# Optimization experiments

Hardware: AMD Instinct MI355X
Metric: run time of the kernel (lower is better)

The kernel has to match this reference:

```python
import jax, jax.numpy as jnp
import numpy as np

D = 512          # input_size (feature dim)
C = 100          # num_classes
N = 2048         # test samples
ALPHA = 0.5      # regularization mixing parameter
SHRINK = 1e-4    # shrinkage_param


def setup_inputs() -> dict:
    key = jax.random.key(0)
    k1, k2, k3, k4, k5 = jax.random.split(key, 5)
    X = jax.random.normal(k1, (N, D), dtype=jnp.float32)
    muK = jax.random.normal(k2, (C, D), dtype=jnp.float32)
    # Per-class covariances: PSD, well-conditioned (like fitted streaming covariances)
    A = jax.random.normal(k3, (C, D, D), dtype=jnp.float32) * 0.05
    SigmaK = jnp.einsum('cij,ckj->cik', A, A) + 0.1 * jnp.eye(D, dtype=jnp.float32)
    B = jax.random.normal(k4, (D, D), dtype=jnp.float32) * 0.05
    Sigma = B @ B.T + 0.1 * jnp.eye(D, dtype=jnp.float32)
    # class counts (all > 0 so every class is active)
    cK = jax.random.uniform(k5, (C,), dtype=jnp.float32, minval=1.0, maxval=1000.0)
    return {"X": X, "muK": muK, "SigmaK": SigmaK, "Sigma": Sigma, "cK": cK}


def reference(X, muK, SigmaK, Sigma, cK):
    # RegSigmaK[k] = alpha * SigmaK[k] + (1-alpha) * Sigma           [C, D, D]
    RegSigmaK = ALPHA * SigmaK + (1.0 - ALPHA) * Sigma[None, :, :]
    # priors (classes with zero count get prior 1, then are masked to -inf below)
    s = jnp.sum(cK)
    prior = jnp.where(cK == 0, 1.0, cK / s)                          # [C]
    # Lambda[k] = pinv((1-sh) * RegSigmaK[k] + sh * I)               [C, D, D]
    eye = jnp.eye(D, dtype=RegSigmaK.dtype)
    Lambda = jnp.linalg.pinv((1.0 - SHRINK) * RegSigmaK + SHRINK * eye)
    # 0.5 * log ||RegSigmaK[k]||_F  (torch.norm default = Frobenius)
    half_lognorm = 0.5 * jnp.log(jnp.linalg.norm(RegSigmaK, axis=(1, 2)))  # [C]
    # batched Mahalanobis quadratic form: (x - mu_k)^T Lambda_k (x - mu_k)
    diff = X[:, None, :] - muK[None, :, :]                           # [N, C, D]
    quad = jnp.einsum('ncd,cde,nce->nc', diff, Lambda, diff)         # [N, C]
    scores = jnp.log(prior)[None, :] - half_lognorm[None, :] - 0.5 * quad
    scores = jnp.where((cK == 0)[None, :], -jnp.inf, scores)
    return scores
```

## Files before the change

kernel.cpp:

```cpp
#include <hip/hip_runtime.h>
#include <math.h>

#define DIM 512
#define NCLS 100
#define NS 2048
#define DD (DIM*DIM)
#define SHRINKV 1e-4f

typedef short bf16x8 __attribute__((ext_vector_type(8)));
typedef short s16x4 __attribute__((ext_vector_type(4)));
typedef float f32x4 __attribute__((ext_vector_type(4)));

static __device__ __forceinline__ short f2bf(float f) {
  unsigned int u = __float_as_uint(f);
  u += 0x7FFFu + ((u >> 16) & 1u);
  return (short)(u >> 16);
}

__global__ __launch_bounds__(256) void prep_kernel(const float* __restrict__ SigmaK,
                                                   const float* __restrict__ Sigma,
                                                   float* __restrict__ M,
                                                   float* __restrict__ aux) {
  int b = blockIdx.x;
  int k = b >> 2, chunk = b & 3;
  const float* Sk = SigmaK + (size_t)k * DD;
  float* Mk = M + (size_t)k * DD;
  int base0 = chunk << 16;
  float fro = 0.f;
  const float oms = 1.0f - SHRINKV;
  for (int it = 0; it < 64; ++it) {
    int idx = base0 + (it << 10) + (threadIdx.x << 2);
    float4 a = *(const float4*)(Sk + idx);
    float4 g = *(const float4*)(Sigma + idx);
    int r = idx >> 9, c = idx & 511;
    float4 reg;
    reg.x = 0.5f*(a.x + g.x); reg.y = 0.5f*(a.y + g.y);
    reg.z = 0.5f*(a.z + g.z); reg.w = 0.5f*(a.w + g.w);
    fro += reg.x*reg.x + reg.y*reg.y + reg.z*reg.z + reg.w*reg.w;
    float4 m;
    m.x = oms*reg.x + ((r == c + 0) ? SHRINKV : 0.f);
    m.y = oms*reg.y + ((r == c + 1) ? SHRINKV : 0.f);
    m.z = oms*reg.z + ((r == c + 2) ? SHRINKV : 0.f);
    m.w = oms*reg.w + ((r == c + 3) ? SHRINKV : 0.f);
    *(float4*)(Mk + idx) = m;
  }
  __shared__ float red[4];
  int lane = threadIdx.x & 63, w = threadIdx.x >> 6;
  for (int o = 32; o > 0; o >>= 1) fro += __shfl_down(fro, o);
  if (lane == 0) red[w] = fro;
  __syncthreads();
  if (threadIdx.x == 0) atomicAdd(&aux[1 + k], red[0] + red[1] + red[2] + red[3]);
}

__global__ __launch_bounds__(256) void fdt_kernel(float* __restrict__ M,
                                                  short* __restrict__ Wb, int p) {
  __shared__ float Llds[64 * 68];
  __shared__ float invT[64 * 68];
  __shared__ float TA[2][64 * 68];
  int kcls = blockIdx.x;
  float* Mk = M + (size_t)kcls * DD;
  short* Wk = Wb + (size_t)kcls * DD;
  int tid = threadIdx.x, lane = tid & 63, wv = tid >> 6;
  int ty = tid >> 4, tx = tid & 15;
  int sr = tid >> 2, sq = (tid & 3) << 4;
  int p0 = p << 6;
  if (wv == 0) {
    float row[64];
    const float* src = Mk + (size_t)(p0 + lane) * DIM + p0;
    #pragma unroll
    for (int c4 = 0; c4 < 64; c4 += 4) {
      float4 v = *(const float4*)(src + c4);
      row[c4] = v.x; row[c4+1] = v.y; row[c4+2] = v.z; row[c4+3] = v.w;
    }
    #pragma unroll
    for (int j = 0; j < 64; ++j) {
      float diagv = __shfl(row[j], j);
      float dv = sqrtf(diagv);
      float rinv = 1.0f / dv;
      float myLj = row[j] * rinv;
      row[j] = myLj;
      #pragma unroll
      for (int c = j + 1; c < 64; ++c)
        row[c] = fmaf(-myLj, __shfl(myLj, c), row[c]);
    }
    #pragma unroll
    for (int c = 0; c < 64; ++c)
      Llds[lane * 68 + c] = (c <= lane) ? row[c] : 0.f;
  }
  __syncthreads();
  if (wv == 0) {
    float w[64];
    #pragma unroll
    for (int r = 0; r < 64; ++r) {
      float s = 0.f;
      #pragma unroll
      for (int kk = 0; kk + 4 <= r; kk += 4) {
        float4 lv = *(const float4*)(Llds + r*68 + kk);
        s += lv.x*w[kk] + lv.y*w[kk+1] + lv.z*w[kk+2] + lv.w*w[kk+3];
      }
      #pragma unroll
      for (int kk = r & ~3; kk < r; ++kk) s += Llds[r*68 + kk] * w[kk];
      float rhs = ((r == lane) ? 1.0f : 0.0f) - s;
      w[r] = rhs / Llds[r*68 + r];
    }
    #pragma unroll
    for (int r = 0; r < 64; ++r) {
      Mk[(size_t)(p0 + r)*DIM + p0 + lane] = w[r];
      Wk[(size_t)(p0 + r)*DIM + p0 + lane] = f2bf(w[r]);
      invT[lane*68 + r] = w[r];
    }
  } else if (p < 7) {
    int w1 = wv - 1;
    int r0 = (w1 == 0) ? 0 : (w1 == 1 ? 22 : 43);
    int r1 = (w1 == 0) ? 22 : (w1 == 1 ? 43 : 64);
    const float* ab = Mk + ((size_t)((p + 1) << 6)) * DIM + p0;
    for (int row = r0; row < r1; ++row)
      TA[0][lane*68 + row] = ab[(size_t)row * DIM + lane];
  }
  __syncthreads();
  int cur = 0;
  for (int i = p + 1; i < 8; ++i) {
    if (i + 1 < 8) {
      const float* a = Mk + (size_t)(((i + 1) << 6) + sr)*DIM + p0 + sq;
      #pragma unroll
      for (int t4 = 0; t4 < 4; ++t4) {
        float4 va = *(const float4*)(a + 4*t4);
        TA[cur^1][(sq+4*t4+0)*68+sr]=va.x; TA[cur^1][(sq+4*t4+1)*68+sr]=va.y;
        TA[cur^1][(sq+4*t4+2)*68+sr]=va.z; TA[cur^1][(sq+4*t4+3)*68+sr]=va.w;
      }
    }
    float acc[4][4];
    #pragma unroll
    for (int a2 = 0; a2 < 4; ++a2)
      #pragma unroll
      for (int b2 = 0; b2 < 4; ++b2) acc[a2][b2] = 0.f;
    #pragma unroll 16
    for (int m = 0; m < 64; ++m) {
      float4 av = *(const float4*)(TA[cur] + m*68 + (ty << 2));
      float4 bv = *(const float4*)(invT + m*68 + (tx << 2));
      float a4[4] = {av.x, av.y, av.z, av.w};
      float b4[4] = {bv.x, bv.y, bv.z, bv.w};
      #pragma unroll
      for (int ir = 0; ir < 4; ++ir)
        #pragma unroll
        for (int ic = 0; ic < 4; ++ic) acc[ir][ic] += a4[ir] * b4[ic];
    }
    #pragma unroll
    for (int q = 0; q < 4; ++q) {
      float4 v; v.x = acc[q][0]; v.y = acc[q][1]; v.z = acc[q][2]; v.w = acc[q][3];
      *(float4*)(Mk + (size_t)((i << 6) + (ty << 2) + q)*DIM + p0 + (tx << 2)) = v;
    }
    __syncthreads();
    cur ^= 1;
  }
}

__global__ __launch_bounds__(256) void syrk_kernel(float* __restrict__ M, int p) {
  __shared__ float TA[64 * 68];
  __shared__ float TB[64 * 68];
  int n = 7 - p;
  int T = n * (n + 1) / 2;
  int cls = blockIdx.x / T;
  int t = blockIdx.x % T;
  int bi = 0;
  while (t > bi) { t -= bi + 1; ++bi; }
  int i = p + 1 + bi, j = p + 1 + t;
  float* Mk = M + (size_t)cls * DD;
  int tid = threadIdx.x;
  int ty = tid >> 4, tx = tid & 15;
  int sr = tid >> 2, sq = (tid & 3) << 4;
  {
    const float* a = Mk + (size_t)((i << 6) + sr)*DIM + (p << 6) + sq;
    const float* b = Mk + (size_t)((j << 6) + sr)*DIM + (p << 6) + sq;
    #pragma unroll
    for (int t4 = 0; t4 < 4; ++t4) {
      float4 va = *(const float4*)(a + 4*t4);
      TA[(sq+4*t4+0)*68+sr]=va.x; TA[(sq+4*t4+1)*68+sr]=va.y;
      TA[(sq+4*t4+2)*68+sr]=va.z; TA[(sq+4*t4+3)*68+sr]=va.w;
      float4 vb = *(const float4*)(b + 4*t4);
      TB[(sq+4*t4+0)*68+sr]=vb.x; TB[(sq+4*t4+1)*68+sr]=vb.y;
      TB[(sq+4*t4+2)*68+sr]=vb.z; TB[(sq+4*t4+3)*68+sr]=vb.w;
    }
  }
  __syncthreads();
  float acc[4][4];
  #pragma unroll
  for (int a = 0; a < 4; ++a)
    #pragma unroll
    for (int b = 0; b < 4; ++b) acc[a][b] = 0.f;
  #pragma unroll 16
  for (int m = 0; m < 64; ++m) {
    float4 av = *(const float4*)(TA + m*68 + (ty << 2));
    float4 bv = *(const float4*)(TB + m*68 + (tx << 2));
    float a4[4] = {av.x, av.y, av.z, av.w};
    float b4[4] = {bv.x, bv.y, bv.z, bv.w};
    #pragma unroll
    for (int ir = 0; ir < 4; ++ir)
      #pragma unroll
      for (int ic = 0; ic < 4; ++ic) acc[ir][ic] += a4[ir] * b4[ic];
  }
  #pragma unroll
  for (int q = 0; q < 4; ++q) {
    float* dst = Mk + (size_t)((i << 6) + (ty << 2) + q)*DIM + (j << 6) + (tx << 2);
    float4 v = *(const float4*)dst;
    v.x -= acc[q][0]; v.y -= acc[q][1]; v.z -= acc[q][2]; v.w -= acc[q][3];
    *(float4*)dst = v;
  }
}

__global__ __launch_bounds__(256) void colsweep_kernel(float* __restrict__ M,
                                                       short* __restrict__ Wb) {
  __shared__ float TL[2][64 * 68];
  __shared__ float TW[2][64 * 68];
  int cls = blockIdx.x / 7;
  int j = blockIdx.x % 7;
  float* Mk = M + (size_t)cls * DD;
  short* Wk = Wb + (size_t)cls * DD;
  int tid = threadIdx.x;
  int ty = tid >> 4, tx = tid & 15;
  int sr = tid >> 2, sq = (tid & 3) << 4;
  for (int i = j + 1; i < 8; ++i) {
    auto stageLW = [&](int k, int buf) {
      const float* a = Mk + (size_t)((i << 6) + sr)*DIM + (k << 6) + sq;
      const float* b = Mk + (size_t)((j << 6) + sr)*DIM + (k << 6) + sq;
      #pragma unroll
      for (int t4 = 0; t4 < 4; ++t4) {
        float4 va = *(const float4*)(a + 4*t4);
        TL[buf][(sq+4*t4+0)*68+sr]=va.x; TL[buf][(sq+4*t4+1)*68+sr]=va.y;
        TL[buf][(sq+4*t4+2)*68+sr]=va.z; TL[buf][(sq+4*t4+3)*68+sr]=va.w;
        *(float4*)(TW[buf] + sr*68 + sq + 4*t4) = *(const float4*)(b + 4*t4);
      }
    };
    float acc[4][4];
    #pragma unroll
    for (int a = 0; a < 4; ++a)
      #pragma unroll
      for (int b = 0; b < 4; ++b) acc[a][b] = 0.f;
    stageLW(j, 0);
    __syncthreads();
    int cur = 0;
    for (int k = j; k < i; ++k) {
      if (k + 1 < i) stageLW(k + 1, cur ^ 1);
      #pragma unroll 16
      for (int m = 0; m < 64; ++m) {
        float4 av = *(const float4*)(TL[cur] + m*68 + (ty << 2));
        float4 bv = *(const float4*)(TW[cur] + m*68 + (tx << 2));
        float a4[4] = {av.x, av.y, av.z, av.w};
        float b4[4] = {bv.x, bv.y, bv.z, bv.w};
        #pragma unroll
        for (int ir = 0; ir < 4; ++ir)
          #pragma unroll
          for (int ic = 0; ic < 4; ++ic) acc[ir][ic] += a4[ir] * b4[ic];
      }
      __syncthreads();
      cur ^= 1;
    }
    #pragma unroll
    for (int q = 0; q < 4; ++q) {
      float4 v; v.x = acc[q][0]; v.y = acc[q][1]; v.z = acc[q][2]; v.w = acc[q][3];
      *(float4*)(TW[0] + ((ty << 2) + q)*68 + (tx << 2)) = v;
    }
    {
      const float* a = Mk + (size_t)((i << 6) + sr)*DIM + (i << 6) + sq;
      #pragma unroll
      for (int t4 = 0; t4 < 4; ++t4) {
        float4 va = *(const float4*)(a + 4*t4);
        TL[0][(sq+4*t4+0)*68+sr]=va.x; TL[0][(sq+4*t4+1)*68+sr]=va.y;
        TL[0][(sq+4*t4+2)*68+sr]=va.z; TL[0][(sq+4*t4+3)*68+sr]=va.w;
      }
    }
    __syncthreads();
    float r2[4][4];
    #pragma unroll
    for (int a = 0; a < 4; ++a)
      #pragma unroll
      for (int b = 0; b < 4; ++b) r2[a][b] = 0.f;
    #pragma unroll 16
    for (int m = 0; m < 64; ++m) {
      float4 av = *(const float4*)(TL[0] + m*68 + (ty << 2));
      float4 bv = *(const float4*)(TW[0] + m*68 + (tx << 2));
      float a4[4] = {av.x, av.y, av.z, av.w};
      float b4[4] = {bv.x, bv.y, bv.z, bv.w};
      #pragma unroll
      for (int ir = 0; ir < 4; ++ir)
        #pragma unroll
        for (int ic = 0; ic < 4; ++ic) r2[ir][ic] += a4[ir] * b4[ic];
    }
    #pragma unroll
    for (int q = 0; q < 4; ++q) {
      int a = (ty << 2) + q;
      float4 v; v.x = -r2[q][0]; v.y = -r2[q][1]; v.z = -r2[q][2]; v.w = -r2[q][3];
      *(float4*)(Mk + (size_t)((j << 6) + a)*DIM + (i << 6) + (tx << 2)) = v;
      s16x4 h;
      h[0] = f2bf(v.x); h[1] = f2bf(v.y); h[2] = f2bf(v.z); h[3] = f2bf(v.w);
      *(s16x4*)(Wk + (size_t)((i << 6) + a)*DIM + (j << 6) + (tx << 2)) = h;
    }
    __syncthreads();
  }
}

__global__ __launch_bounds__(256) void score_kernel(const float* __restrict__ X,
                                                    const float* __restrict__ muK,
                                                    const float* __restrict__ cK,
                                                    const short* __restrict__ W,
                                                    const float* __restrict__ aux,
                                                    float* __restrict__ out) {
  __shared__ __align__(16) char WB4[4][8192];
  __shared__ float sred[4];
  int bid = blockIdx.x;
  int wg = ((bid & 7) * 400) + (bid >> 3);
  int kc = wg >> 5;
  int n0 = (wg & 31) << 6;
  int tid = threadIdx.x;
  int lane = tid & 63, wv = tid >> 6;
  const short* Wk = W + (size_t)kc * DD;
  const float* mu = muK + (size_t)kc * DIM;
  int r16 = lane & 15;
  int k8 = (lane >> 4) << 3;
  int arow = (wv << 4) + r16;

  int lrow = lane >> 3;
  int lcolel = ((lane & 7) ^ lrow) << 3;

  constexpr int SJT[36] = {0,1,1, 2,3,2,3,2,3,3, 4,5,4,5,4,5,4,5,4,5,5,
                           6,7,6,7,6,7,6,7,6,7,6,7,6,7,7};
  constexpr int SDC[36] = {0,0,1, 0,0,1,1,2,2,3, 0,0,1,1,2,2,3,3,4,4,5,
                           0,0,1,1,2,2,3,3,4,4,5,5,6,6,7};

  bf16x8 af[8][2];
  #pragma unroll
  for (int dc = 0; dc < 8; ++dc) {
    #pragma unroll
    for (int ks = 0; ks < 2; ++ks) {
      int col = (dc << 6) + (ks << 5) + k8;
      const float* xp = X + (size_t)(n0 + arow)*DIM + col;
      float4 x0 = *(const float4*)xp;
      float4 x1 = *(const float4*)(xp + 4);
      float4 m0 = *(const float4*)(mu + col);
      float4 m1 = *(const float4*)(mu + col + 4);
      bf16x8 h;
      h[0]=f2bf(x0.x-m0.x); h[1]=f2bf(x0.y-m0.y); h[2]=f2bf(x0.z-m0.z); h[3]=f2bf(x0.w-m0.w);
      h[4]=f2bf(x1.x-m1.x); h[5]=f2bf(x1.y-m1.y); h[6]=f2bf(x1.z-m1.z); h[7]=f2bf(x1.w-m1.w);
      af[dc][ks] = h;
    }
  }

  auto issue = [&](int s) {
    const int b = s & 3;
    const int rbase = SJT[s] << 6;
    const int cc = (SDC[s] << 6) + lcolel;
    #pragma unroll
    for (int q = 0; q < 2; ++q) {
      const short* g = Wk + (size_t)(rbase + (q << 5) + (wv << 3) + lrow)*DIM + cc;
      __builtin_amdgcn_global_load_lds(
          (const __attribute__((address_space(1))) void*)g,
          (__attribute__((address_space(3))) void*)(WB4[b] + (q << 12) + (wv << 10)),
          16, 0, 0);
    }
  };

  float qp[4] = {0.f, 0.f, 0.f, 0.f};
  f32x4 acc[2][4];
  #pragma unroll
  for (int a = 0; a < 2; ++a)
    #pragma unroll
    for (int jj = 0; jj < 4; ++jj) { acc[a][jj][0]=0.f; acc[a][jj][1]=0.f; acc[a][jj][2]=0.f; acc[a][jj][3]=0.f; }

  issue(0);
  issue(1);
  #pragma unroll
  for (int s = 0; s < 36; ++s) {
    const int jt = SJT[s], dc = SDC[s];
    if (s + 2 < 36) issue(s + 2);
    if (s < 34)      asm volatile("s_waitcnt vmcnt(4)" ::: "memory");
    else if (s == 34) asm volatile("s_waitcnt vmcnt(2)" ::: "memory");
    else              asm volatile("s_waitcnt vmcnt(0)" ::: "memory");
    __builtin_amdgcn_s_barrier();
    __builtin_amdgcn_sched_barrier(0);
    __builtin_amdgcn_s_setprio(1);
    #pragma unroll
    for (int ks = 0; ks < 2; ++ks) {
      #pragma unroll
      for (int jj = 0; jj < 4; ++jj) {
        int brow = (jj << 4) + r16;
        bf16x8 bfr = *(const bf16x8*)((const char*)WB4[s & 3] +
                     (((brow << 7) + (((ks << 5) + k8) << 1)) ^ ((brow & 7) << 4)));
        acc[jt & 1][jj] = __builtin_amdgcn_mfma_f32_16x16x32_bf16(af[dc][ks], bfr, acc[jt & 1][jj], 0, 0, 0);
      }
    }
    __builtin_amdgcn_s_setprio(0);
    if (s == 2 || s == 9 || s == 20 || s == 35) {
      #pragma unroll
      for (int a = 0; a < 2; ++a)
        #pragma unroll
        for (int jj = 0; jj < 4; ++jj)
          #pragma unroll
          for (int r = 0; r < 4; ++r) {
            float y = acc[a][jj][r]; qp[r] += y * y;
            acc[a][jj][r] = 0.f;
          }
    }
  }
  #pragma unroll
  for (int r = 0; r < 4; ++r) {
    qp[r] += __shfl_xor(qp[r], 1);
    qp[r] += __shfl_xor(qp[r], 2);
    qp[r] += __shfl_xor(qp[r], 4);
    qp[r] += __shfl_xor(qp[r], 8);
  }
  {
    float v = (tid < NCLS) ? cK[tid] : 0.f;
    #pragma unroll
    for (int o = 32; o > 0; o >>= 1) v += __shfl_xor(v, o);
    if (lane == 0) sred[wv] = v;
  }
  __syncthreads();
  float sumck = sred[0] + sred[1] + sred[2] + sred[3];
  float ck = cK[kc];
  float base;
  if (ck == 0.f) base = -INFINITY;
  else base = logf(ck) - logf(sumck) - 0.25f * logf(aux[1 + kc]);
  if ((lane & 15) == 0) {
    int nbase = n0 + (wv << 4) + ((lane >> 4) << 2);
    #pragma unroll
    for (int r = 0; r < 4; ++r)
      out[(size_t)(nbase + r)*NCLS + kc] = base - 0.5f * qp[r];
  }
}

extern "C" void kernel_launch(void* const* d_in, const int* in_sizes, int n_in,
                              void* d_out, int out_size, void* d_ws, size_t ws_size,
                              hipStream_t stream) {
  (void)in_sizes; (void)n_in; (void)out_size; (void)ws_size;
  const float* X      = (const float*)d_in[0];
  const float* muK    = (const float*)d_in[1];
  const float* SigmaK = (const float*)d_in[2];
  const float* Sigma  = (const float*)d_in[3];
  const float* cK     = (const float*)d_in[4];
  float* out = (float*)d_out;
  char* ws = (char*)d_ws;
  float* M   = (float*)ws;
  short* W   = (short*)(ws + (size_t)NCLS * DD * 4);
  float* aux = (float*)(ws + (size_t)NCLS * DD * 6);

  hipMemsetAsync(aux, 0, (1 + NCLS) * sizeof(float), stream);
  prep_kernel<<<400, 256, 0, stream>>>(SigmaK, Sigma, M, aux);
  for (int p = 0; p < 8; ++p) {
    fdt_kernel<<<NCLS, 256, 0, stream>>>(M, W, p);
    int n = 7 - p;
    if (n > 0) syrk_kernel<<<NCLS * (n * (n + 1) / 2), 256, 0, stream>>>(M, p);
  }
  colsweep_kernel<<<NCLS * 7, 256, 0, stream>>>(M, W);
  score_kernel<<<NCLS * 32, 256, 0, stream>>>(X, muK, cK, W, aux, out);
}
```

Measured before the change: 871.2 us.

## Restructure blocked Cholesky into parallel TRSM and fused SYRK/diag-factor kernels

Splits the old per-class fdt kernel, which factored the diagonal block and ran the panel solve serially in one 256-thread block, into a fully parallel trsm kernel over panel blocks. The first panel block also computes the next diagonal block's SYRK update. A combo kernel then runs the remaining SYRK tiles alongside the next diagonal factorization, taking that serial step off the critical path. Adds an XCD-aware block index swizzle for L2 locality. The diagonal-factor blocks in the combo kernel use only 64 of their 256 threads.

```diff
diff --git a/kernel.cpp b/kernel.cpp
--- a/kernel.cpp
+++ b/kernel.cpp
@@ -15,6 +15,12 @@
   unsigned int u = __float_as_uint(f);
   u += 0x7FFFu + ((u >> 16) & 1u);
   return (short)(u >> 16);
+}
+
+static __device__ __forceinline__ int xcd_swz(int bid, int nwg) {
+  int xcd = bid & 7, idx = bid >> 3;
+  int q = nwg >> 3, r = nwg & 7;
+  return (xcd < r ? xcd * (q + 1) : r * (q + 1) + (xcd - r) * q) + idx;
 }
 
 __global__ __launch_bounds__(256) void prep_kernel(const float* __restrict__ SigmaK,
@@ -52,126 +58,74 @@
   if (threadIdx.x == 0) atomicAdd(&aux[1 + k], red[0] + red[1] + red[2] + red[3]);
 }
 
-__global__ __launch_bounds__(256) void fdt_kernel(float* __restrict__ M,
-                                                  short* __restrict__ Wb, int p) {
+static __device__ __forceinline__ void fdiag_dev(float* __restrict__ Mk,
+                                                 short* __restrict__ Wk,
+                                                 int p0, int lane,
+                                                 float* __restrict__ Llds) {
+  float row[64];
+  const float* src = Mk + (size_t)(p0 + lane) * DIM + p0;
+  #pragma unroll
+  for (int c4 = 0; c4 < 64; c4 += 4) {
+    float4 v = *(const float4*)(src + c4);
+    row[c4] = v.x; row[c4+1] = v.y; row[c4+2] = v.z; row[c4+3] = v.w;
+  }
+  #pragma unroll
+  for (int j = 0; j < 64; ++j) {
+    float diagv = __shfl(row[j], j);
+    float dv = sqrtf(diagv);
+    float rinv = 1.0f / dv;
+    float myLj = row[j] * rinv;
+    row[j] = myLj;
+    #pragma unroll
+    for (int c = j + 1; c < 64; ++c)
+      row[c] = fmaf(-myLj, __shfl(myLj, c), row[c]);
+  }
+  #pragma unroll
+  for (int c = 0; c < 64; ++c)
+    Llds[lane * 68 + c] = (c <= lane) ? row[c] : 0.f;
+  float w[64];
+  #pragma unroll
+  for (int r = 0; r < 64; ++r) {
+    float s = 0.f;
+    #pragma unroll
+    for (int kk = 0; kk + 4 <= r; kk += 4) {
+      float4 lv = *(const float4*)(Llds + r*68 + kk);
+      s += lv.x*w[kk] + lv.y*w[kk+1] + lv.z*w[kk+2] + lv.w*w[kk+3];
+    }
+    #pragma unroll
+    for (int kk = r & ~3; kk < r; ++kk) s += Llds[r*68 + kk] * w[kk];
+    float rhs = ((r == lane) ? 1.0f : 0.0f) - s;
+    w[r] = rhs / Llds[r*68 + r];
+  }
+  #pragma unroll
+  for (int r = 0; r < 64; ++r) {
+    Mk[(size_t)(p0 + r)*DIM + p0 + lane] = w[r];
+    Wk[(size_t)(p0 + r)*DIM + p0 + lane] = f2bf(w[r]);
+  }
+}
+
+__global__ __launch_bounds__(64) void fdiag_kernel(float* __restrict__ M,
+                                                   short* __restrict__ Wb) {
   __shared__ float Llds[64 * 68];
-  __shared__ float invT[64 * 68];
-  __shared__ float TA[2][64 * 68];
-  int kcls = blockIdx.x;
-  float* Mk = M + (size_t)kcls * DD;
-  short* Wk = Wb + (size_t)kcls * DD;
-  int tid = threadIdx.x, lane = tid & 63, wv = tid >> 6;
-  int ty = tid >> 4, tx = tid & 15;
-  int sr = tid >> 2, sq = (tid & 3) << 4;
-  int p0 = p << 6;
-  if (wv == 0) {
-    float row[64];
-    const float* src = Mk + (size_t)(p0 + lane) * DIM + p0;
-    #pragma unroll
-    for (int c4 = 0; c4 < 64; c4 += 4) {
-      float4 v = *(const float4*)(src + c4);
-      row[c4] = v.x; row[c4+1] = v.y; row[c4+2] = v.z; row[c4+3] = v.w;
-    }
-    #pragma unroll
-    for (int j = 0; j < 64; ++j) {
-      float diagv = __shfl(row[j], j);
-      float dv = sqrtf(diagv);
-      float rinv = 1.0f / dv;
-      float myLj = row[j] * rinv;
-      row[j] = myLj;
-      #pragma unroll
-      for (int c = j + 1; c < 64; ++c)
-        row[c] = fmaf(-myLj, __shfl(myLj, c), row[c]);
-    }
-    #pragma unroll
-    for (int c = 0; c < 64; ++c)
-      Llds[lane * 68 + c] = (c <= lane) ? row[c] : 0.f;
-  }
-  __syncthreads();
-  if (wv == 0) {
-    float w[64];
-    #pragma unroll
-    for (int r = 0; r < 64; ++r) {
-      float s = 0.f;
-      #pragma unroll
-      for (int kk = 0; kk + 4 <= r; kk += 4) {
-        float4 lv = *(const float4*)(Llds + r*68 + kk);
-        s += lv.x*w[kk] + lv.y*w[kk+1] + lv.z*w[kk+2] + lv.w*w[kk+3];
-      }
-      #pragma unroll
-      for (int kk = r & ~3; kk < r; ++kk) s += Llds[r*68 + kk] * w[kk];
-      float rhs = ((r == lane) ? 1.0f : 0.0f) - s;
-      w[r] = rhs / Llds[r*68 + r];
-    }
-    #pragma unroll
-    for (int r = 0; r < 64; ++r) {
-      Mk[(size_t)(p0 + r)*DIM + p0 + lane] = w[r];
-      Wk[(size_t)(p0 + r)*DIM + p0 + lane] = f2bf(w[r]);
-      invT[lane*68 + r] = w[r];
-    }
-  } else if (p < 7) {
-    int w1 = wv - 1;
-    int r0 = (w1 == 0) ? 0 : (w1 == 1 ? 22 : 43);
-    int r1 = (w1 == 0) ? 22 : (w1 == 1 ? 43 : 64);
-    const float* ab = Mk + ((size_t)((p + 1) << 6)) * DIM + p0;
-    for (int row = r0; row < r1; ++row)
-      TA[0][lane*68 + row] = ab[(size_t)row * DIM + lane];
-  }
-  __syncthreads();
-  int cur = 0;
-  for (int i = p + 1; i < 8; ++i) {
-    if (i + 1 < 8) {
-      const float* a = Mk + (size_t)(((i + 1) << 6) + sr)*DIM + p0 + sq;
-      #pragma unroll
-      for (int t4 = 0; t4 < 4; ++t4) {
-        float4 va = *(const float4*)(a + 4*t4);
-        TA[cur^1][(sq+4*t4+0)*68+sr]=va.x; TA[cur^1][(sq+4*t4+1)*68+sr]=va.y;
-        TA[cur^1][(sq+4*t4+2)*68+sr]=va.z; TA[cur^1][(sq+4*t4+3)*68+sr]=va.w;
-      }
-    }
-    float acc[4][4];
-    #pragma unroll
-    for (int a2 = 0; a2 < 4; ++a2)
-      #pragma unroll
-      for (int b2 = 0; b2 < 4; ++b2) acc[a2][b2] = 0.f;
-    #pragma unroll 16
-    for (int m = 0; m < 64; ++m) {
-      float4 av = *(const float4*)(TA[cur] + m*68 + (ty << 2));
-      float4 bv = *(const float4*)(invT + m*68 + (tx << 2));
-      float a4[4] = {av.x, av.y, av.z, av.w};
-      float b4[4] = {bv.x, bv.y, bv.z, bv.w};
-      #pragma unroll
-      for (int ir = 0; ir < 4; ++ir)
-        #pragma unroll
-        for (int ic = 0; ic < 4; ++ic) acc[ir][ic] += a4[ir] * b4[ic];
-    }
-    #pragma unroll
-    for (int q = 0; q < 4; ++q) {
-      float4 v; v.x = acc[q][0]; v.y = acc[q][1]; v.z = acc[q][2]; v.w = acc[q][3];
-      *(float4*)(Mk + (size_t)((i << 6) + (ty << 2) + q)*DIM + p0 + (tx << 2)) = v;
-    }
-    __syncthreads();
-    cur ^= 1;
-  }
-}
-
-__global__ __launch_bounds__(256) void syrk_kernel(float* __restrict__ M, int p) {
+  fdiag_dev(M + (size_t)blockIdx.x * DD, Wb + (size_t)blockIdx.x * DD,
+            0, threadIdx.x, Llds);
+}
+
+__global__ __launch_bounds__(256) void trsm_kernel(float* __restrict__ M, int p) {
   __shared__ float TA[64 * 68];
   __shared__ float TB[64 * 68];
   int n = 7 - p;
-  int T = n * (n + 1) / 2;
-  int cls = blockIdx.x / T;
-  int t = blockIdx.x % T;
-  int bi = 0;
-  while (t > bi) { t -= bi + 1; ++bi; }
-  int i = p + 1 + bi, j = p + 1 + t;
+  int wg = xcd_swz(blockIdx.x, NCLS * n);
+  int cls = wg / n, bi = wg % n;
+  int i = p + 1 + bi;
   float* Mk = M + (size_t)cls * DD;
   int tid = threadIdx.x;
   int ty = tid >> 4, tx = tid & 15;
   int sr = tid >> 2, sq = (tid & 3) << 4;
+  int p0 = p << 6;
   {
-    const float* a = Mk + (size_t)((i << 6) + sr)*DIM + (p << 6) + sq;
-    const float* b = Mk + (size_t)((j << 6) + sr)*DIM + (p << 6) + sq;
+    const float* a = Mk + (size_t)((i << 6) + sr)*DIM + p0 + sq;
+    const float* b = Mk + (size_t)(p0 + sr)*DIM + p0 + sq;
     #pragma unroll
     for (int t4 = 0; t4 < 4; ++t4) {
       float4 va = *(const float4*)(a + 4*t4);
@@ -185,6 +139,100 @@
   __syncthreads();
   float acc[4][4];
   #pragma unroll
+  for (int a2 = 0; a2 < 4; ++a2)
+    #pragma unroll
+    for (int b2 = 0; b2 < 4; ++b2) acc[a2][b2] = 0.f;
+  #pragma unroll 16
+  for (int m = 0; m < 64; ++m) {
+    float4 av = *(const float4*)(TA + m*68 + (ty << 2));
+    float4 bv = *(const float4*)(TB + m*68 + (tx << 2));
+    float a4[4] = {av.x, av.y, av.z, av.w};
+    float b4[4] = {bv.x, bv.y, bv.z, bv.w};
+    #pragma unroll
+    for (int ir = 0; ir < 4; ++ir)
+      #pragma unroll
+      for (int ic = 0; ic < 4; ++ic) acc[ir][ic] += a4[ir] * b4[ic];
+  }
+  #pragma unroll
+  for (int q = 0; q < 4; ++q) {
+    float4 v; v.x = acc[q][0]; v.y = acc[q][1]; v.z = acc[q][2]; v.w = acc[q][3];
+    *(float4*)(Mk + (size_t)((i << 6) + (ty << 2) + q)*DIM + p0 + (tx << 2)) = v;
+  }
+  if (bi == 0) {
+    __syncthreads();
+    #pragma unroll
+    for (int q = 0; q < 4; ++q)
+      #pragma unroll
+      for (int cc = 0; cc < 4; ++cc)
+        TA[((tx << 2) + cc)*68 + (ty << 2) + q] = acc[q][cc];
+    __syncthreads();
+    float s2[4][4];
+    #pragma unroll
+    for (int a2 = 0; a2 < 4; ++a2)
+      #pragma unroll
+      for (int b2 = 0; b2 < 4; ++b2) s2[a2][b2] = 0.f;
+    #pragma unroll 16
+    for (int m = 0; m < 64; ++m) {
+      float4 av = *(const float4*)(TA + m*68 + (ty << 2));
+      float4 bv = *(const float4*)(TA + m*68 + (tx << 2));
+      float a4[4] = {av.x, av.y, av.z, av.w};
+      float b4[4] = {bv.x, bv.y, bv.z, bv.w};
+      #pragma unroll
+      for (int ir = 0; ir < 4; ++ir)
+        #pragma unroll
+        for (int ic = 0; ic < 4; ++ic) s2[ir][ic] += a4[ir] * b4[ic];
+    }
+    int d0 = (p + 1) << 6;
+    #pragma unroll
+    for (int q = 0; q < 4; ++q) {
+      float* dst = Mk + (size_t)(d0 + (ty << 2) + q)*DIM + d0 + (tx << 2);
+      float4 v = *(const float4*)dst;
+      v.x -= s2[q][0]; v.y -= s2[q][1]; v.z -= s2[q][2]; v.w -= s2[q][3];
+      *(float4*)dst = v;
+    }
+  }
+}
+
+__global__ __launch_bounds__(256) void combo_kernel(float* __restrict__ M,
+                                                    short* __restrict__ Wb, int p) {
+  __shared__ float TA[64 * 68];
+  __shared__ float TB[64 * 68];
+  int n = 7 - p;
+  int T = n * (n + 1) / 2;
+  int nsyrk = NCLS * (T - 1);
+  int wg = xcd_swz(blockIdx.x, nsyrk + NCLS);
+  int tid = threadIdx.x;
+  if (wg >= nsyrk) {
+    int cls = wg - nsyrk;
+    if (tid < 64)
+      fdiag_dev(M + (size_t)cls * DD, Wb + (size_t)cls * DD,
+                (p + 1) << 6, tid, TA);
+    return;
+  }
+  int cls = wg / (T - 1);
+  int t = wg % (T - 1) + 1;
+  int bi = 0;
+  while (t > bi) { t -= bi + 1; ++bi; }
+  int i = p + 1 + bi, j = p + 1 + t;
+  float* Mk = M + (size_t)cls * DD;
+  int ty = tid >> 4, tx = tid & 15;
+  int sr = tid >> 2, sq = (tid & 3) << 4;
+  {
+    const float* a = Mk + (size_t)((i << 6) + sr)*DIM + (p << 6) + sq;
+    const float* b = Mk + (size_t)((j << 6) + sr)*DIM + (p << 6) + sq;
+    #pragma unroll
+    for (int t4 = 0; t4 < 4; ++t4) {
+      float4 va = *(const float4*)(a + 4*t4);
+      TA[(sq+4*t4+0)*68+sr]=va.x; TA[(sq+4*t4+1)*68+sr]=va.y;
+      TA[(sq+4*t4+2)*68+sr]=va.z; TA[(sq+4*t4+3)*68+sr]=va.w;
+      float4 vb = *(const float4*)(b + 4*t4);
+      TB[(sq+4*t4+0)*68+sr]=vb.x; TB[(sq+4*t4+1)*68+sr]=vb.y;
+      TB[(sq+4*t4+2)*68+sr]=vb.z; TB[(sq+4*t4+3)*68+sr]=vb.w;
+    }
+  }
+  __syncthreads();
+  float acc[4][4];
+  #pragma unroll
   for (int a = 0; a < 4; ++a)
     #pragma unroll
     for (int b = 0; b < 4; ++b) acc[a][b] = 0.f;
@@ -212,8 +260,9 @@
                                                        short* __restrict__ Wb) {
   __shared__ float TL[2][64 * 68];
   __shared__ float TW[2][64 * 68];
-  int cls = blockIdx.x / 7;
-  int j = blockIdx.x % 7;
+  int wg = xcd_swz(blockIdx.x, NCLS * 7);
+  int cls = wg / 7;
+  int j = wg % 7;
   float* Mk = M + (size_t)cls * DD;
   short* Wk = Wb + (size_t)cls * DD;
   int tid = threadIdx.x;
@@ -445,10 +494,12 @@
 
   hipMemsetAsync(aux, 0, (1 + NCLS) * sizeof(float), stream);
   prep_kernel<<<400, 256, 0, stream>>>(SigmaK, Sigma, M, aux);
-  for (int p = 0; p < 8; ++p) {
-    fdt_kernel<<<NCLS, 256, 0, stream>>>(M, W, p);
+  fdiag_kernel<<<NCLS, 64, 0, stream>>>(M, W);
+  for (int p = 0; p < 7; ++p) {
     int n = 7 - p;
-    if (n > 0) syrk_kernel<<<NCLS * (n * (n + 1) / 2), 256, 0, stream>>>(M, p);
+    int T = n * (n + 1) / 2;
+    trsm_kernel<<<NCLS * n, 256, 0, stream>>>(M, p);
+    combo_kernel<<<NCLS * (T - 1) + NCLS, 256, 0, stream>>>(M, W, p);
   }
   colsweep_kernel<<<NCLS * 7, 256, 0, stream>>>(M, W);
   score_kernel<<<NCLS * 32, 256, 0, stream>>>(X, muK, cK, W, aux, out);
```

Measured after the change: 798.5 us. 1.09x faster.

## Fuse blocked Cholesky, trailing update and inverse sweep into one per-class kernel

Applied to the files above, without the earlier changes.

Replaces the 15 separate fdt/syrk launches and the colsweep kernel with a single factor_kernel that runs one block per class through all eight panel steps. The whole transposed panel is kept in a large LDS buffer so the trailing SYRK update reuses it instead of reloading tiles from global memory, and the column sweep for the inverse is interleaved per panel. This removes launch overhead and global round trips between stages. In exchange there are only 100 blocks, so most of the GPU sits idle and the serial work per block grows, and the large LDS footprint lowers occupancy.

```diff
diff --git a/kernel.cpp b/kernel.cpp
--- a/kernel.cpp
+++ b/kernel.cpp
@@ -52,250 +52,224 @@
   if (threadIdx.x == 0) atomicAdd(&aux[1 + k], red[0] + red[1] + red[2] + red[3]);
 }
 
-__global__ __launch_bounds__(256) void fdt_kernel(float* __restrict__ M,
-                                                  short* __restrict__ Wb, int p) {
-  __shared__ float Llds[64 * 68];
+static __device__ __forceinline__ void fdiag_dev(float* __restrict__ Mk,
+                                                 short* __restrict__ Wk,
+                                                 int p0, int lane,
+                                                 float* __restrict__ Llds,
+                                                 float* __restrict__ invT) {
+  float row[64];
+  const float* src = Mk + (size_t)(p0 + lane) * DIM + p0;
+  #pragma unroll
+  for (int c4 = 0; c4 < 64; c4 += 4) {
+    float4 v = *(const float4*)(src + c4);
+    row[c4] = v.x; row[c4+1] = v.y; row[c4+2] = v.z; row[c4+3] = v.w;
+  }
+  #pragma unroll
+  for (int j = 0; j < 64; ++j) {
+    float diagv = __shfl(row[j], j);
+    float dv = sqrtf(diagv);
+    float rinv = 1.0f / dv;
+    float myLj = row[j] * rinv;
+    row[j] = myLj;
+    #pragma unroll
+    for (int c = j + 1; c < 64; ++c)
+      row[c] = fmaf(-myLj, __shfl(myLj, c), row[c]);
+  }
+  #pragma unroll
+  for (int c = 0; c < 64; ++c)
+    Llds[lane * 68 + c] = (c <= lane) ? row[c] : 0.f;
+  float w[64];
+  #pragma unroll
+  for (int r = 0; r < 64; ++r) {
+    float s = 0.f;
+    #pragma unroll
+    for (int kk = 0; kk + 4 <= r; kk += 4) {
+      float4 lv = *(const float4*)(Llds + r*68 + kk);
+      s += lv.x*w[kk] + lv.y*w[kk+1] + lv.z*w[kk+2] + lv.w*w[kk+3];
+    }
+    #pragma unroll
+    for (int kk = r & ~3; kk < r; ++kk) s += Llds[r*68 + kk] * w[kk];
+    float rhs = ((r == lane) ? 1.0f : 0.0f) - s;
+    w[r] = rhs / Llds[r*68 + r];
+  }
+  #pragma unroll
+  for (int r = 0; r < 64; ++r) {
+    Mk[(size_t)(p0 + r)*DIM + p0 + lane] = w[r];
+    Wk[(size_t)(p0 + r)*DIM + p0 + lane] = f2bf(w[r]);
+    invT[lane*68 + r] = w[r];
+  }
+}
+
+__global__ __launch_bounds__(256) void factor_kernel(float* __restrict__ M,
+                                                     short* __restrict__ Wb) {
+  __shared__ float panT[64 * 452];
   __shared__ float invT[64 * 68];
-  __shared__ float TA[2][64 * 68];
-  int kcls = blockIdx.x;
-  float* Mk = M + (size_t)kcls * DD;
-  short* Wk = Wb + (size_t)kcls * DD;
-  int tid = threadIdx.x, lane = tid & 63, wv = tid >> 6;
-  int ty = tid >> 4, tx = tid & 15;
-  int sr = tid >> 2, sq = (tid & 3) << 4;
-  int p0 = p << 6;
-  if (wv == 0) {
-    float row[64];
-    const float* src = Mk + (size_t)(p0 + lane) * DIM + p0;
-    #pragma unroll
-    for (int c4 = 0; c4 < 64; c4 += 4) {
-      float4 v = *(const float4*)(src + c4);
-      row[c4] = v.x; row[c4+1] = v.y; row[c4+2] = v.z; row[c4+3] = v.w;
-    }
-    #pragma unroll
-    for (int j = 0; j < 64; ++j) {
-      float diagv = __shfl(row[j], j);
-      float dv = sqrtf(diagv);
-      float rinv = 1.0f / dv;
-      float myLj = row[j] * rinv;
-      row[j] = myLj;
-      #pragma unroll
-      for (int c = j + 1; c < 64; ++c)
-        row[c] = fmaf(-myLj, __shfl(myLj, c), row[c]);
-    }
-    #pragma unroll
-    for (int c = 0; c < 64; ++c)
-      Llds[lane * 68 + c] = (c <= lane) ? row[c] : 0.f;
-  }
-  __syncthreads();
-  if (wv == 0) {
-    float w[64];
-    #pragma unroll
-    for (int r = 0; r < 64; ++r) {
-      float s = 0.f;
-      #pragma unroll
-      for (int kk = 0; kk + 4 <= r; kk += 4) {
-        float4 lv = *(const float4*)(Llds + r*68 + kk);
-        s += lv.x*w[kk] + lv.y*w[kk+1] + lv.z*w[kk+2] + lv.w*w[kk+3];
-      }
-      #pragma unroll
-      for (int kk = r & ~3; kk < r; ++kk) s += Llds[r*68 + kk] * w[kk];
-      float rhs = ((r == lane) ? 1.0f : 0.0f) - s;
-      w[r] = rhs / Llds[r*68 + r];
-    }
-    #pragma unroll
-    for (int r = 0; r < 64; ++r) {
-      Mk[(size_t)(p0 + r)*DIM + p0 + lane] = w[r];
-      Wk[(size_t)(p0 + r)*DIM + p0 + lane] = f2bf(w[r]);
-      invT[lane*68 + r] = w[r];
-    }
-  } else if (p < 7) {
-    int w1 = wv - 1;
-    int r0 = (w1 == 0) ? 0 : (w1 == 1 ? 22 : 43);
-    int r1 = (w1 == 0) ? 22 : (w1 == 1 ? 43 : 64);
-    const float* ab = Mk + ((size_t)((p + 1) << 6)) * DIM + p0;
-    for (int row = r0; row < r1; ++row)
-      TA[0][lane*68 + row] = ab[(size_t)row * DIM + lane];
-  }
-  __syncthreads();
-  int cur = 0;
-  for (int i = p + 1; i < 8; ++i) {
-    if (i + 1 < 8) {
-      const float* a = Mk + (size_t)(((i + 1) << 6) + sr)*DIM + p0 + sq;
-      #pragma unroll
-      for (int t4 = 0; t4 < 4; ++t4) {
-        float4 va = *(const float4*)(a + 4*t4);
-        TA[cur^1][(sq+4*t4+0)*68+sr]=va.x; TA[cur^1][(sq+4*t4+1)*68+sr]=va.y;
-        TA[cur^1][(sq+4*t4+2)*68+sr]=va.z; TA[cur^1][(sq+4*t4+3)*68+sr]=va.w;
-      }
-    }
-    float acc[4][4];
-    #pragma unroll
-    for (int a2 = 0; a2 < 4; ++a2)
-      #pragma unroll
-      for (int b2 = 0; b2 < 4; ++b2) acc[a2][b2] = 0.f;
-    #pragma unroll 16
-    for (int m = 0; m < 64; ++m) {
-      float4 av = *(const float4*)(TA[cur] + m*68 + (ty << 2));
-      float4 bv = *(const float4*)(invT + m*68 + (tx << 2));
-      float a4[4] = {av.x, av.y, av.z, av.w};
-      float b4[4] = {bv.x, bv.y, bv.z, bv.w};
-      #pragma unroll
-      for (int ir = 0; ir < 4; ++ir)
-        #pragma unroll
-        for (int ic = 0; ic < 4; ++ic) acc[ir][ic] += a4[ir] * b4[ic];
-    }
-    #pragma unroll
-    for (int q = 0; q < 4; ++q) {
-      float4 v; v.x = acc[q][0]; v.y = acc[q][1]; v.z = acc[q][2]; v.w = acc[q][3];
-      *(float4*)(Mk + (size_t)((i << 6) + (ty << 2) + q)*DIM + p0 + (tx << 2)) = v;
-    }
+  __shared__ float TB[64 * 68];
+  float* Mk = M + (size_t)blockIdx.x * DD;
+  short* Wk = Wb + (size_t)blockIdx.x * DD;
+  const int tid = threadIdx.x, wv = tid >> 6;
+  const int ty = tid >> 4, tx = tid & 15;
+  const int sr = tid >> 2, sq = (tid & 3) << 4;
+
+  for (int p = 0; p < 8; ++p) {
+    const int p0 = p << 6;
+    const int n = 7 - p;
+    const int H = n << 6;
     __syncthreads();
-    cur ^= 1;
-  }
-}
-
-__global__ __launch_bounds__(256) void syrk_kernel(float* __restrict__ M, int p) {
-  __shared__ float TA[64 * 68];
-  __shared__ float TB[64 * 68];
-  int n = 7 - p;
-  int T = n * (n + 1) / 2;
-  int cls = blockIdx.x / T;
-  int t = blockIdx.x % T;
-  int bi = 0;
-  while (t > bi) { t -= bi + 1; ++bi; }
-  int i = p + 1 + bi, j = p + 1 + t;
-  float* Mk = M + (size_t)cls * DD;
-  int tid = threadIdx.x;
-  int ty = tid >> 4, tx = tid & 15;
-  int sr = tid >> 2, sq = (tid & 3) << 4;
-  {
-    const float* a = Mk + (size_t)((i << 6) + sr)*DIM + (p << 6) + sq;
-    const float* b = Mk + (size_t)((j << 6) + sr)*DIM + (p << 6) + sq;
-    #pragma unroll
-    for (int t4 = 0; t4 < 4; ++t4) {
-      float4 va = *(const float4*)(a + 4*t4);
-      TA[(sq+4*t4+0)*68+sr]=va.x; TA[(sq+4*t4+1)*68+sr]=va.y;
-      TA[(sq+4*t4+2)*68+sr]=va.z; TA[(sq+4*t4+3)*68+sr]=va.w;
-      float4 vb = *(const float4*)(b + 4*t4);
-      TB[(sq+4*t4+0)*68+sr]=vb.x; TB[(sq+4*t4+1)*68+sr]=vb.y;
-      TB[(sq+4*t4+2)*68+sr]=vb.z; TB[(sq+4*t4+3)*68+sr]=vb.w;
-    }
-  }
-  __syncthreads();
-  float acc[4][4];
-  #pragma unroll
-  for (int a = 0; a < 4; ++a)
-    #pragma unroll
-    for (int b = 0; b < 4; ++b) acc[a][b] = 0.f;
-  #pragma unroll 16
-  for (int m = 0; m < 64; ++m) {
-    float4 av = *(const float4*)(TA + m*68 + (ty << 2));
-    float4 bv = *(const float4*)(TB + m*68 + (tx << 2));
-    float a4[4] = {av.x, av.y, av.z, av.w};
-    float b4[4] = {bv.x, bv.y, bv.z, bv.w};
-    #pragma unroll
-    for (int ir = 0; ir < 4; ++ir)
-      #pragma unroll
-      for (int ic = 0; ic < 4; ++ic) acc[ir][ic] += a4[ir] * b4[ic];
-  }
-  #pragma unroll
-  for (int q = 0; q < 4; ++q) {
-    float* dst = Mk + (size_t)((i << 6) + (ty << 2) + q)*DIM + (j << 6) + (tx << 2);
-    float4 v = *(const float4*)dst;
-    v.x -= acc[q][0]; v.y -= acc[q][1]; v.z -= acc[q][2]; v.w -= acc[q][3];
-    *(float4*)dst = v;
-  }
-}
-
-__global__ __launch_bounds__(256) void colsweep_kernel(float* __restrict__ M,
-                                                       short* __restrict__ Wb) {
-  __shared__ float TL[2][64 * 68];
-  __shared__ float TW[2][64 * 68];
-  int cls = blockIdx.x / 7;
-  int j = blockIdx.x % 7;
-  float* Mk = M + (size_t)cls * DD;
-  short* Wk = Wb + (size_t)cls * DD;
-  int tid = threadIdx.x;
-  int ty = tid >> 4, tx = tid & 15;
-  int sr = tid >> 2, sq = (tid & 3) << 4;
-  for (int i = j + 1; i < 8; ++i) {
-    auto stageLW = [&](int k, int buf) {
-      const float* a = Mk + (size_t)((i << 6) + sr)*DIM + (k << 6) + sq;
-      const float* b = Mk + (size_t)((j << 6) + sr)*DIM + (k << 6) + sq;
-      #pragma unroll
-      for (int t4 = 0; t4 < 4; ++t4) {
-        float4 va = *(const float4*)(a + 4*t4);
-        TL[buf][(sq+4*t4+0)*68+sr]=va.x; TL[buf][(sq+4*t4+1)*68+sr]=va.y;
-        TL[buf][(sq+4*t4+2)*68+sr]=va.z; TL[buf][(sq+4*t4+3)*68+sr]=va.w;
-        *(float4*)(TW[buf] + sr*68 + sq + 4*t4) = *(const float4*)(b + 4*t4);
-      }
-    };
-    float acc[4][4];
-    #pragma unroll
-    for (int a = 0; a < 4; ++a)
-      #pragma unroll
-      for (int b = 0; b < 4; ++b) acc[a][b] = 0.f;
-    stageLW(j, 0);
+    if (wv == 0) {
+      fdiag_dev(Mk, Wk, p0, tid, TB, invT);
+    } else if (n > 0) {
+      for (int it = tid - 64; it < (n << 8); it += 192) {
+        int i = it % H;
+        int c16 = (it / H) << 4;
+        const float* src = Mk + (size_t)(p0 + 64 + i) * DIM + p0 + c16;
+        float4 v0 = *(const float4*)(src + 0);
+        float4 v1 = *(const float4*)(src + 4);
+        float4 v2 = *(const float4*)(src + 8);
+        float4 v3 = *(const float4*)(src + 12);
+        float* dst = panT + i;
+        dst[(c16+ 0)*452]=v0.x; dst[(c16+ 1)*452]=v0.y; dst[(c16+ 2)*452]=v0.z; dst[(c16+ 3)*452]=v0.w;
+        dst[(c16+ 4)*452]=v1.x; dst[(c16+ 5)*452]=v1.y; dst[(c16+ 6)*452]=v1.z; dst[(c16+ 7)*452]=v1.w;
+        dst[(c16+ 8)*452]=v2.x; dst[(c16+ 9)*452]=v2.y; dst[(c16+10)*452]=v2.z; dst[(c16+11)*452]=v2.w;
+        dst[(c16+12)*452]=v3.x; dst[(c16+13)*452]=v3.y; dst[(c16+14)*452]=v3.z; dst[(c16+15)*452]=v3.w;
+      }
+    }
     __syncthreads();
-    int cur = 0;
-    for (int k = j; k < i; ++k) {
-      if (k + 1 < i) stageLW(k + 1, cur ^ 1);
+    for (int ib = 0; ib < n; ++ib) {
+      const int boff = ib << 6;
+      float l2[4][4];
+      #pragma unroll
+      for (int a2 = 0; a2 < 4; ++a2)
+        #pragma unroll
+        for (int b2 = 0; b2 < 4; ++b2) l2[a2][b2] = 0.f;
       #pragma unroll 16
       for (int m = 0; m < 64; ++m) {
-        float4 av = *(const float4*)(TL[cur] + m*68 + (ty << 2));
-        float4 bv = *(const float4*)(TW[cur] + m*68 + (tx << 2));
+        float4 av = *(const float4*)(&panT[m*452 + boff + (ty << 2)]);
+        float4 bv = *(const float4*)(&invT[m*68 + (tx << 2)]);
         float a4[4] = {av.x, av.y, av.z, av.w};
         float b4[4] = {bv.x, bv.y, bv.z, bv.w};
         #pragma unroll
         for (int ir = 0; ir < 4; ++ir)
           #pragma unroll
-          for (int ic = 0; ic < 4; ++ic) acc[ir][ic] += a4[ir] * b4[ic];
+          for (int ic = 0; ic < 4; ++ic) l2[ir][ic] += a4[ir] * b4[ic];
       }
       __syncthreads();
-      cur ^= 1;
-    }
-    #pragma unroll
-    for (int q = 0; q < 4; ++q) {
-      float4 v; v.x = acc[q][0]; v.y = acc[q][1]; v.z = acc[q][2]; v.w = acc[q][3];
-      *(float4*)(TW[0] + ((ty << 2) + q)*68 + (tx << 2)) = v;
-    }
-    {
-      const float* a = Mk + (size_t)((i << 6) + sr)*DIM + (i << 6) + sq;
-      #pragma unroll
-      for (int t4 = 0; t4 < 4; ++t4) {
-        float4 va = *(const float4*)(a + 4*t4);
-        TL[0][(sq+4*t4+0)*68+sr]=va.x; TL[0][(sq+4*t4+1)*68+sr]=va.y;
-        TL[0][(sq+4*t4+2)*68+sr]=va.z; TL[0][(sq+4*t4+3)*68+sr]=va.w;
+      #pragma unroll
+      for (int q = 0; q < 4; ++q) {
+        float4 v; v.x = l2[q][0]; v.y = l2[q][1]; v.z = l2[q][2]; v.w = l2[q][3];
+        *(float4*)(Mk + (size_t)(p0 + 64 + boff + (ty << 2) + q)*DIM + p0 + (tx << 2)) = v;
+        #pragma unroll
+        for (int cc = 0; cc < 4; ++cc)
+          panT[((tx << 2) + cc)*452 + boff + (ty << 2) + q] = l2[q][cc];
       }
     }
     __syncthreads();
-    float r2[4][4];
-    #pragma unroll
-    for (int a = 0; a < 4; ++a)
-      #pragma unroll
-      for (int b = 0; b < 4; ++b) r2[a][b] = 0.f;
-    #pragma unroll 16
-    for (int m = 0; m < 64; ++m) {
-      float4 av = *(const float4*)(TL[0] + m*68 + (ty << 2));
-      float4 bv = *(const float4*)(TW[0] + m*68 + (tx << 2));
-      float a4[4] = {av.x, av.y, av.z, av.w};
-      float b4[4] = {bv.x, bv.y, bv.z, bv.w};
-      #pragma unroll
-      for (int ir = 0; ir < 4; ++ir)
-        #pragma unroll
-        for (int ic = 0; ic < 4; ++ic) r2[ir][ic] += a4[ir] * b4[ic];
-    }
-    #pragma unroll
-    for (int q = 0; q < 4; ++q) {
-      int a = (ty << 2) + q;
-      float4 v; v.x = -r2[q][0]; v.y = -r2[q][1]; v.z = -r2[q][2]; v.w = -r2[q][3];
-      *(float4*)(Mk + (size_t)((j << 6) + a)*DIM + (i << 6) + (tx << 2)) = v;
-      s16x4 h;
-      h[0] = f2bf(v.x); h[1] = f2bf(v.y); h[2] = f2bf(v.z); h[3] = f2bf(v.w);
-      *(s16x4*)(Wk + (size_t)((i << 6) + a)*DIM + (j << 6) + (tx << 2)) = h;
-    }
-    __syncthreads();
+    for (int bi = 0; bi < n; ++bi) {
+      for (int bj = 0; bj <= bi; ++bj) {
+        float* cb = Mk + (size_t)(p0 + 64 + (bi << 6) + (ty << 2))*DIM
+                       + p0 + 64 + (bj << 6) + (tx << 2);
+        float4 c0 = *(const float4*)(cb + 0*DIM);
+        float4 c1 = *(const float4*)(cb + 1*DIM);
+        float4 c2 = *(const float4*)(cb + 2*DIM);
+        float4 c3 = *(const float4*)(cb + 3*DIM);
+        float acc[4][4];
+        #pragma unroll
+        for (int a2 = 0; a2 < 4; ++a2)
+          #pragma unroll
+          for (int b2 = 0; b2 < 4; ++b2) acc[a2][b2] = 0.f;
+        const int oi = bi << 6, oj = bj << 6;
+        #pragma unroll 16
+        for (int m = 0; m < 64; ++m) {
+          float4 av = *(const float4*)(&panT[m*452 + oi + (ty << 2)]);
+          float4 bv = *(const float4*)(&panT[m*452 + oj + (tx << 2)]);
+          float a4[4] = {av.x, av.y, av.z, av.w};
+          float b4[4] = {bv.x, bv.y, bv.z, bv.w};
+          #pragma unroll
+          for (int ir = 0; ir < 4; ++ir)
+            #pragma unroll
+            for (int ic = 0; ic < 4; ++ic) acc[ir][ic] += a4[ir] * b4[ic];
+        }
+        c0.x -= acc[0][0]; c0.y -= acc[0][1]; c0.z -= acc[0][2]; c0.w -= acc[0][3];
+        c1.x -= acc[1][0]; c1.y -= acc[1][1]; c1.z -= acc[1][2]; c1.w -= acc[1][3];
+        c2.x -= acc[2][0]; c2.y -= acc[2][1]; c2.z -= acc[2][2]; c2.w -= acc[2][3];
+        c3.x -= acc[3][0]; c3.y -= acc[3][1]; c3.z -= acc[3][2]; c3.w -= acc[3][3];
+        *(float4*)(cb + 0*DIM) = c0;
+        *(float4*)(cb + 1*DIM) = c1;
+        *(float4*)(cb + 2*DIM) = c2;
+        *(float4*)(cb + 3*DIM) = c3;
+      }
+    }
+    for (int j = 0; j < p; ++j) {
+      __syncthreads();
+      auto stageLW = [&](int k, int buf) {
+        const float* a = Mk + (size_t)(p0 + sr)*DIM + (k << 6) + sq;
+        const float* b = Mk + (size_t)((j << 6) + sr)*DIM + (k << 6) + sq;
+        #pragma unroll
+        for (int t4 = 0; t4 < 4; ++t4) {
+          float4 va = *(const float4*)(a + 4*t4);
+          panT[buf*4352 + (sq+4*t4+0)*68+sr]=va.x;
+          panT[buf*4352 + (sq+4*t4+1)*68+sr]=va.y;
+          panT[buf*4352 + (sq+4*t4+2)*68+sr]=va.z;
+          panT[buf*4352 + (sq+4*t4+3)*68+sr]=va.w;
+          *(float4*)(&panT[(2+buf)*4352 + sr*68 + sq + 4*t4]) = *(const float4*)(b + 4*t4);
+        }
+      };
+      float acc[4][4];
+      #pragma unroll
+      for (int a = 0; a < 4; ++a)
+        #pragma unroll
+        for (int b = 0; b < 4; ++b) acc[a][b] = 0.f;
+      stageLW(j, 0);
+      __syncthreads();
+      int cur = 0;
+      for (int k = j; k < p; ++k) {
+        if (k + 1 < p) stageLW(k + 1, cur ^ 1);
+        #pragma unroll 16
+        for (int m = 0; m < 64; ++m) {
+          float4 av = *(const float4*)(&panT[cur*4352 + m*68 + (ty << 2)]);
+          float4 bv = *(const float4*)(&panT[(2+cur)*4352 + m*68 + (tx << 2)]);
+          float a4[4] = {av.x, av.y, av.z, av.w};
+          float b4[4] = {bv.x, bv.y, bv.z, bv.w};
+          #pragma unroll
+          for (int ir = 0; ir < 4; ++ir)
+            #pragma unroll
+            for (int ic = 0; ic < 4; ++ic) acc[ir][ic] += a4[ir] * b4[ic];
+        }
+        __syncthreads();
+        cur ^= 1;
+      }
+      #pragma unroll
+      for (int q = 0; q < 4; ++q) {
+        float4 v; v.x = acc[q][0]; v.y = acc[q][1]; v.z = acc[q][2]; v.w = acc[q][3];
+        *(float4*)(&panT[2*4352 + ((ty << 2) + q)*68 + (tx << 2)]) = v;
+      }
+      __syncthreads();
+      float r2[4][4];
+      #pragma unroll
+      for (int a = 0; a < 4; ++a)
+        #pragma unroll
+        for (int b = 0; b < 4; ++b) r2[a][b] = 0.f;
+      #pragma unroll 16
+      for (int m = 0; m < 64; ++m) {
+        float4 av = *(const float4*)(&invT[m*68 + (ty << 2)]);
+        float4 bv = *(const float4*)(&panT[2*4352 + m*68 + (tx << 2)]);
+        float a4[4] = {av.x, av.y, av.z, av.w};
+        float b4[4] = {bv.x, bv.y, bv.z, bv.w};
+        #pragma unroll
+        for (int ir = 0; ir < 4; ++ir)
+          #pragma unroll
+          for (int ic = 0; ic < 4; ++ic) r2[ir][ic] += a4[ir] * b4[ic];
+      }
+      #pragma unroll
+      for (int q = 0; q < 4; ++q) {
+        int a = (ty << 2) + q;
+        float4 v; v.x = -r2[q][0]; v.y = -r2[q][1]; v.z = -r2[q][2]; v.w = -r2[q][3];
+        *(float4*)(Mk + (size_t)((j << 6) + a)*DIM + p0 + (tx << 2)) = v;
+        s16x4 h;
+        h[0] = f2bf(v.x); h[1] = f2bf(v.y); h[2] = f2bf(v.z); h[3] = f2bf(v.w);
+        *(s16x4*)(Wk + (size_t)(p0 + a)*DIM + (j << 6) + (tx << 2)) = h;
+      }
+    }
   }
 }
 
@@ -443,13 +417,8 @@
   short* W   = (short*)(ws + (size_t)NCLS * DD * 4);
   float* aux = (float*)(ws + (size_t)NCLS * DD * 6);
 
-  hipMemsetAsync(aux, 0, (1 + NCLS) * sizeof(float), stream);
+  (void)hipMemsetAsync(aux, 0, (1 + NCLS) * sizeof(float), stream);
   prep_kernel<<<400, 256, 0, stream>>>(SigmaK, Sigma, M, aux);
-  for (int p = 0; p < 8; ++p) {
-    fdt_kernel<<<NCLS, 256, 0, stream>>>(M, W, p);
-    int n = 7 - p;
-    if (n > 0) syrk_kernel<<<NCLS * (n * (n + 1) / 2), 256, 0, stream>>>(M, p);
-  }
-  colsweep_kernel<<<NCLS * 7, 256, 0, stream>>>(M, W);
+  factor_kernel<<<NCLS, 256, 0, stream>>>(M, W);
   score_kernel<<<NCLS * 32, 256, 0, stream>>>(X, muK, cK, W, aux, out);
 }
```

Result: slower. 1.700 ms (+95.1%).
